# Kernel optimization log

Hardware: AMD Instinct MI355X
Metric: run time of the kernel (lower is better)

The kernel has to match this reference:

```python
import jax, jax.numpy as jnp
import numpy as np

B, C, H, W = 4, 512, 56, 56
G, K = 16, 3
P = K * K
GC = C // G
DWK = 3
PAD = 1
OFFSET_SCALE = 1.0


def setup_inputs():
    key = jax.random.key(0)
    ks = jax.random.split(key, 10)

    def w(i, shape, sc=0.02):
        return jax.random.normal(ks[i], shape, jnp.float32) * sc

    return {
        "x": jax.random.normal(ks[0], (B, C, H, W), jnp.float32),
        "w_in": w(1, (C, C)), "b_in": jnp.zeros((C,), jnp.float32),
        "w_dw": w(2, (DWK, DWK, 1, C)), "b_dw": jnp.zeros((C,), jnp.float32),
        "ln_g": jnp.ones((C,), jnp.float32), "ln_b": jnp.zeros((C,), jnp.float32),
        "w_off": w(3, (C, G * P * 2)), "b_off": jnp.zeros((G * P * 2,), jnp.float32),
        "w_mask": w(4, (C, G * P)), "b_mask": jnp.zeros((G * P,), jnp.float32),
        "w_out": w(5, (C, C)), "b_out": jnp.zeros((C,), jnp.float32),
        "bn_g": jnp.ones((C,), jnp.float32), "bn_b": jnp.zeros((C,), jnp.float32),
        "bn_m": w(6, (C,), 0.1), "bn_v": jnp.abs(w(7, (C,), 0.1)) + 1.0,
    }


def _dcnv3_core(xp, offset, mask):
    """xp: [B,H,W,C]; offset: [B,H,W,G*P*2]; mask (softmaxed over P): [B,H,W,G,P]."""
    xpad = jnp.pad(xp, ((0, 0), (PAD, PAD), (PAD, PAD), (0, 0)))
    Hin, Win = H + 2 * PAD, W + 2 * PAD
    # normalized reference points (output-location centers in padded input coords)
    ref_x = (jnp.arange(W, dtype=jnp.float32) + 0.5 + (K - 1) // 2) / Win
    ref_y = (jnp.arange(H, dtype=jnp.float32) + 0.5 + (K - 1) // 2) / Hin
    # dilation grid, kx-major / ky-minor flattening (matches InternImage core)
    k = jnp.arange(K, dtype=jnp.float32) - (K - 1) // 2
    gx = jnp.repeat(k, K) / Win  # [P]
    gy = jnp.tile(k, K) / Hin    # [P]
    off = offset.reshape(B, H, W, G, P, 2)
    lx = ref_x[None, None, :, None, None] + gx * OFFSET_SCALE + off[..., 0] * OFFSET_SCALE / Win
    ly = ref_y[None, :, None, None, None] + gy * OFFSET_SCALE + off[..., 1] * OFFSET_SCALE / Hin
    # grid_sample semantics, align_corners=False, zero padding
    px = lx * Win - 0.5
    py = ly * Hin - 0.5
    x0f = jnp.floor(px)
    y0f = jnp.floor(py)
    tx = px - x0f
    ty = py - y0f
    x0 = x0f.astype(jnp.int32)
    y0 = y0f.astype(jnp.int32)
    flat = xpad.reshape(B, Hin * Win * G, GC)
    gidx = jnp.arange(G)[None, None, :, None]

    def corner(fb, yi, xi):
        valid = (yi >= 0) & (yi < Hin) & (xi >= 0) & (xi < Win)
        idx = (jnp.clip(yi, 0, Hin - 1) * Win + jnp.clip(xi, 0, Win - 1)) * G + gidx
        return jnp.take(fb, idx, axis=0) * valid[..., None]  # [H,W,G,P,GC]

    def sample_one(fb, y0b, x0b, tyb, txb):
        w00 = ((1 - tyb) * (1 - txb))[..., None]
        w01 = ((1 - tyb) * txb)[..., None]
        w10 = (tyb * (1 - txb))[..., None]
        w11 = (tyb * txb)[..., None]
        return (corner(fb, y0b, x0b) * w00 + corner(fb, y0b, x0b + 1) * w01
                + corner(fb, y0b + 1, x0b) * w10 + corner(fb, y0b + 1, x0b + 1) * w11)

    samp = jax.vmap(sample_one)(flat, y0, x0, ty, tx)  # [B,H,W,G,P,GC]
    return jnp.einsum('bhwgpc,bhwgp->bhwgc', samp, mask).reshape(B, H, W, C)


def reference(x, w_in, b_in, w_dw, b_dw, ln_g, ln_b, w_off, b_off, w_mask, b_mask, w_out, b_out, bn_g, bn_b, bn_m, bn_v):
    xh = jnp.transpose(x, (0, 2, 3, 1))  # NCHW -> NHWC
    xp = xh @ w_in + b_in                # input_proj
    # offset/mask branch: depthwise conv + LayerNorm(channels) + GELU
    x1 = jax.lax.conv_general_dilated(xh, w_dw, (1, 1), 'SAME', feature_group_count=C,
                                      dimension_numbers=('NHWC', 'HWIO', 'NHWC')) + b_dw
    mu = x1.mean(-1, keepdims=True)
    var = x1.var(-1, keepdims=True)
    x1 = (x1 - mu) / jnp.sqrt(var + 1e-6) * ln_g + ln_b
    x1 = jax.nn.gelu(x1, approximate=False)
    offset = x1 @ w_off + b_off
    mask = jax.nn.softmax((x1 @ w_mask + b_mask).reshape(B, H, W, G, P), axis=-1)
    y = _dcnv3_core(xp, offset, mask)
    y = y @ w_out + b_out                # output_proj
    y = jnp.transpose(y, (0, 3, 1, 2))   # NHWC -> NCHW
    # BatchNorm2d (inference: running stats) + SiLU
    y = (y - bn_m[:, None, None]) / jnp.sqrt(bn_v[:, None, None] + 1e-5) * bn_g[:, None, None] + bn_b[:, None, None]
    return jax.nn.silu(y)
```

## Files before the change

### kernel.cpp

```cpp
#include <hip/hip_runtime.h>
#include <cmath>

constexpr int B_ = 4, C_ = 512, H_ = 56, W_ = 56;
constexpr int HW_ = H_ * W_;
constexpr int NPIX = B_ * HW_;
constexpr int G_ = 16, P_ = 9;
constexpr int NMSK = G_ * P_;
constexpr int GEMM_BLOCKS = 1568;
constexpr int TRANS_BLOCKS = (HW_ / 32) * (C_ / 32) * B_;
constexpr int PREP_BLOCKS = 16 * 16 * 3;

typedef __attribute__((ext_vector_type(8))) short short8;
typedef __attribute__((ext_vector_type(4))) float f32x4;

__device__ __forceinline__ float b2f(ushort u) {
    union { unsigned int i; float f; } v; v.i = (unsigned int)u << 16; return v.f;
}
__device__ __forceinline__ ushort f2b(float f) {
    unsigned int x = __float_as_uint(f);
    unsigned int r = (x + 0x7fffu + ((x >> 16) & 1u)) >> 16;
    return (ushort)r;
}
__device__ __forceinline__ void gload16(const ushort* g, ushort* l) {
    __builtin_amdgcn_global_load_lds(
        (const __attribute__((address_space(1))) unsigned int*)g,
        (__attribute__((address_space(3))) unsigned int*)l, 16, 0, 0);
}

union GemmSMem {
    struct { ushort As[64 * 64]; ushort Bs[64 * 64]; } s;
    float eb[64 * 67];
};

__global__ __launch_bounds__(256) void pre_kernel(
    const float* __restrict__ x, ushort* __restrict__ xh,
    const float* __restrict__ w_in, const float* __restrict__ w_off,
    const float* __restrict__ w_mask, const float* __restrict__ w_out,
    const float* __restrict__ b_off, const float* __restrict__ b_mask,
    ushort* __restrict__ wtA, ushort* __restrict__ wtOM, ushort* __restrict__ wtO,
    float* __restrict__ bOM)
{
    __shared__ float tile[32][33];
    int bid = blockIdx.x;
    int tx = threadIdx.x, ty = threadIdx.y;
    if (bid < TRANS_BLOCKS) {
        int bx = bid % 98;
        int rem = bid / 98;
        int by = rem % 16;
        int bz = rem / 16;
        int hw0 = bx * 32, c0 = by * 32;
        const float* ib = x + (size_t)bz * C_ * HW_;
        #pragma unroll
        for (int i = ty; i < 32; i += 8)
            tile[i][tx] = ib[(size_t)(c0 + i) * HW_ + hw0 + tx];
        __syncthreads();
        ushort* ob = xh + (size_t)bz * HW_ * C_;
        #pragma unroll
        for (int i = ty; i < 32; i += 8)
            ob[(size_t)(hw0 + i) * C_ + c0 + tx] = f2b(tile[tx][i]);
    } else {
        int p = bid - TRANS_BLOCKS;
        int px = p % 16;
        int py = (p / 16) % 16;
        int pz = p / 256;
        int k0 = px * 32;
        int n0 = py * 32;
        for (int i = ty; i < 32; i += 8) {
            int k = k0 + i, n = n0 + tx;
            float v;
            if (pz == 0) v = w_in[k * 512 + n];
            else if (pz == 1) v = w_out[k * 512 + n];
            else v = (n < 288) ? w_off[k * 288 + n]
                               : (n < 432 ? w_mask[k * 144 + (n - 288)] : 0.f);
            tile[i][tx] = v;
        }
        __syncthreads();
        ushort* dst = (pz == 0) ? wtA : (pz == 1 ? wtO : wtOM);
        for (int i = ty; i < 32; i += 8)
            dst[(size_t)(n0 + i) * 512 + k0 + tx] = f2b(tile[tx][i]);
        if (pz == 2 && px == 0 && py == 0) {
            int t = ty * 32 + tx;
            for (int tt = t; tt < 512; tt += 256)
                bOM[tt] = (tt < 288) ? b_off[tt] : (tt < 432 ? b_mask[tt - 288] : 0.f);
        }
    }
}

template <int MODE>
__device__ __forceinline__ void gemm_body(
    ushort* __restrict__ As, ushort* __restrict__ Bs, float* __restrict__ ebf,
    int wgid, const ushort* __restrict__ A, const ushort* __restrict__ Bt,
    const float* __restrict__ bias, void* __restrict__ Cout,
    const float* __restrict__ bng, const float* __restrict__ bnb,
    const float* __restrict__ bnm, const float* __restrict__ bnv)
{
    int tid = threadIdx.x;
    int lane = tid & 63, wid = tid >> 6;
    int row0 = (wgid >> 3) * 64, col0 = (wgid & 7) * 64;
    int wm = wid >> 1, wn = wid & 1;

    f32x4 acc[2][2] = {};

    int lr = lane >> 3;
    int sc = (lane & 7) ^ lr;

    for (int k0 = 0; k0 < 512; k0 += 64) {
        if (k0) __syncthreads();
        #pragma unroll
        for (int i = 0; i < 2; i++) {
            int s = wid * 2 + i;
            gload16(A + (size_t)(row0 + s * 8 + lr) * 512 + k0 + sc * 8, &As[s * 512]);
            gload16(Bt + (size_t)(col0 + s * 8 + lr) * 512 + k0 + sc * 8, &Bs[s * 512]);
        }
        __syncthreads();
        #pragma unroll
        for (int ks = 0; ks < 2; ks++) {
            short8 af[2], bf[2];
            #pragma unroll
            for (int mi = 0; mi < 2; mi++) {
                int r = wm * 32 + mi * 16 + (lane & 15);
                int c = ((lane >> 4) + ks * 4) ^ (r & 7);
                af[mi] = *(const short8*)((const char*)As + r * 128 + c * 16);
            }
            #pragma unroll
            for (int ni = 0; ni < 2; ni++) {
                int r = wn * 32 + ni * 16 + (lane & 15);
                int c = ((lane >> 4) + ks * 4) ^ (r & 7);
                bf[ni] = *(const short8*)((const char*)Bs + r * 128 + c * 16);
            }
            #pragma unroll
            for (int mi = 0; mi < 2; mi++)
                #pragma unroll
                for (int ni = 0; ni < 2; ni++)
                    acc[mi][ni] = __builtin_amdgcn_mfma_f32_16x16x32_bf16(
                        af[mi], bf[ni], acc[mi][ni], 0, 0, 0);
        }
    }

    if constexpr (MODE == 2) {
        __syncthreads();
        #pragma unroll
        for (int ni = 0; ni < 2; ni++) {
            int cl = wn * 32 + ni * 16 + (lane & 15);
            int col = col0 + cl;
            float bv = bias[col];
            float inv = rsqrtf(bnv[col] + 1e-5f);
            float bsc = bng[col] * inv;
            float bsh = bnb[col] - bnm[col] * bsc;
            int rl = (lane >> 4) * 4;
            #pragma unroll
            for (int mi = 0; mi < 2; mi++)
                #pragma unroll
                for (int r = 0; r < 4; r++) {
                    float val = acc[mi][ni][r] + bv;
                    float t2 = val * bsc + bsh;
                    float s = t2 / (1.f + expf(-t2));
                    ebf[cl * 67 + wm * 32 + mi * 16 + rl + r] = s;
                }
        }
        __syncthreads();
        int bb = row0 / HW_;
        int hw0 = row0 - bb * HW_;
        float* ob = (float*)Cout + (size_t)bb * C_ * HW_ + hw0 + lane;
        #pragma unroll
        for (int it = 0; it < 16; it++) {
            int chan = it * 4 + wid;
            ob[(size_t)(col0 + chan) * HW_] = ebf[chan * 67 + lane];
        }
    } else {
        #pragma unroll
        for (int ni = 0; ni < 2; ni++) {
            int col = col0 + wn * 32 + ni * 16 + (lane & 15);
            float bv = bias[col];
            #pragma unroll
            for (int mi = 0; mi < 2; mi++) {
                int rowb = row0 + wm * 32 + mi * 16 + (lane >> 4) * 4;
                #pragma unroll
                for (int r = 0; r < 4; r++) {
                    float val = acc[mi][ni][r] + bv;
                    if constexpr (MODE == 0)
                        ((float*)Cout)[(size_t)(rowb + r) * 512 + col] = val;
                    else
                        ((ushort*)Cout)[(size_t)(rowb + r) * 512 + col] = f2b(val);
                }
            }
        }
    }
}

template <int MODE, bool SKIPC7 = false>
__global__ __launch_bounds__(256) void mfma_gemm_kernel(
    const ushort* __restrict__ A, const ushort* __restrict__ Bt,
    const float* __restrict__ bias, void* __restrict__ Cout,
    const float* __restrict__ bng, const float* __restrict__ bnb,
    const float* __restrict__ bnm, const float* __restrict__ bnv)
{
    __shared__ GemmSMem sm;
    int bid = blockIdx.x;
    int wgid = (bid & 7) * (GEMM_BLOCKS / 8) + (bid >> 3);
    if (SKIPC7 && (wgid & 7) == 7) return;
    gemm_body<MODE>(sm.s.As, sm.s.Bs, sm.eb, wgid,
                    A, Bt, bias, Cout, bng, bnb, bnm, bnv);
}

__device__ __forceinline__ void dwln_body(
    int bid, const ushort* __restrict__ xh, const float* __restrict__ wdw,
    const float* __restrict__ bdw, const float* __restrict__ lng,
    const float* __restrict__ lnb, ushort* __restrict__ x1)
{
    int tid = threadIdx.x;
    int wid = tid >> 6, lane = tid & 63;
    int j = (bid & 7) * (NPIX / 32) + (bid >> 3);
    int n = j * 4 + wid;
    int b = n / HW_, hw = n % HW_;
    int h = hw / W_, w = hw % W_;
    int c0 = lane * 8;
    const ushort* base = xh + (size_t)b * HW_ * C_ + c0;

    uint4 nb[9];
    #pragma unroll
    for (int ky = 0; ky < 3; ky++)
        #pragma unroll
        for (int kx = 0; kx < 3; kx++) {
            int hh = h + ky - 1, ww = w + kx - 1;
            bool ok = (hh >= 0) & (hh < H_) & (ww >= 0) & (ww < W_);
            nb[ky * 3 + kx] = ok ? *(const uint4*)(base + ((size_t)hh * W_ + ww) * C_)
                                 : make_uint4(0u, 0u, 0u, 0u);
        }

    float acc[8];
    {
        float4 b0 = *(const float4*)&bdw[c0];
        float4 b1 = *(const float4*)&bdw[c0 + 4];
        acc[0] = b0.x; acc[1] = b0.y; acc[2] = b0.z; acc[3] = b0.w;
        acc[4] = b1.x; acc[5] = b1.y; acc[6] = b1.z; acc[7] = b1.w;
    }
    #pragma unroll
    for (int p = 0; p < 9; p++) {
        float4 w0 = *(const float4*)&wdw[p * C_ + c0];
        float4 w1 = *(const float4*)&wdw[p * C_ + c0 + 4];
        float wv[8] = {w0.x, w0.y, w0.z, w0.w, w1.x, w1.y, w1.z, w1.w};
        unsigned int u[4] = {nb[p].x, nb[p].y, nb[p].z, nb[p].w};
        #pragma unroll
        for (int q = 0; q < 4; q++) {
            float lo = __uint_as_float(u[q] << 16);
            float hi = __uint_as_float(u[q] & 0xffff0000u);
            acc[2 * q]     += wv[2 * q]     * lo;
            acc[2 * q + 1] += wv[2 * q + 1] * hi;
        }
    }

    float s1 = 0.f, s2 = 0.f;
    #pragma unroll
    for (int q = 0; q < 8; q++) { s1 += acc[q]; s2 += acc[q] * acc[q]; }
    #pragma unroll
    for (int o = 32; o > 0; o >>= 1) {
        s1 += __shfl_xor(s1, o);
        s2 += __shfl_xor(s2, o);
    }
    float mean = s1 * (1.f / 512.f);
    float var = s2 * (1.f / 512.f) - mean * mean;
    float inv = rsqrtf(var + 1e-6f);

    float4 g0 = *(const float4*)&lng[c0];
    float4 g1 = *(const float4*)&lng[c0 + 4];
    float4 e0 = *(const float4*)&lnb[c0];
    float4 e1 = *(const float4*)&lnb[c0 + 4];
    float gv[8] = {g0.x, g0.y, g0.z, g0.w, g1.x, g1.y, g1.z, g1.w};
    float ev[8] = {e0.x, e0.y, e0.z, e0.w, e1.x, e1.y, e1.z, e1.w};
    unsigned int outw[4];
    #pragma unroll
    for (int q = 0; q < 4; q++) {
        float t0 = (acc[2 * q]     - mean) * inv * gv[2 * q]     + ev[2 * q];
        float t1 = (acc[2 * q + 1] - mean) * inv * gv[2 * q + 1] + ev[2 * q + 1];
        float ge0 = 0.5f * t0 * (1.f + erff(t0 * 0.70710678118654752f));
        float ge1 = 0.5f * t1 * (1.f + erff(t1 * 0.70710678118654752f));
        outw[q] = (unsigned int)f2b(ge0) | ((unsigned int)f2b(ge1) << 16);
    }
    *(uint4*)&x1[(size_t)n * C_ + c0] = make_uint4(outw[0], outw[1], outw[2], outw[3]);
}

__global__ __launch_bounds__(256) void g1_dwln_kernel(
    const ushort* __restrict__ xh, const ushort* __restrict__ wtA,
    const float* __restrict__ b_in, ushort* __restrict__ xpb,
    const float* __restrict__ wdw, const float* __restrict__ bdw,
    const float* __restrict__ lng, const float* __restrict__ lnb,
    ushort* __restrict__ x1)
{
    __shared__ GemmSMem sm;
    int bid = blockIdx.x;
    if (bid < GEMM_BLOCKS) {
        int wgid = (bid & 7) * (GEMM_BLOCKS / 8) + (bid >> 3);
        gemm_body<1>(sm.s.As, sm.s.Bs, sm.eb, wgid,
                     xh, wtA, b_in, xpb, nullptr, nullptr, nullptr, nullptr);
    } else {
        dwln_body(bid - GEMM_BLOCKS, xh, wdw, bdw, lng, lnb, x1);
    }
}

__global__ __launch_bounds__(256) void dcn_sample_kernel(
    const ushort* __restrict__ xp, const ushort* __restrict__ om,
    ushort* __restrict__ y1)
{
    __shared__ float slog[NMSK];
    __shared__ float sw4[NMSK][4];
    __shared__ int   sa4[NMSK][4];
    int bid = blockIdx.x;
    int n = (bid & 7) * (NPIX / 8) + (bid >> 3);
    int b = n / HW_, hw = n % HW_;
    int h = hw / W_, w = hw % W_;
    int tid = threadIdx.x;
    const ushort* omp = om + (size_t)n * 512;

    if (tid < NMSK) slog[tid] = b2f(omp[288 + tid]);
    __syncthreads();
    if (tid < G_) {
        float mx = -1e30f;
        #pragma unroll
        for (int p = 0; p < P_; p++) mx = fmaxf(mx, slog[tid * P_ + p]);
        float e[P_], s = 0.f;
        #pragma unroll
        for (int p = 0; p < P_; p++) { e[p] = expf(slog[tid * P_ + p] - mx); s += e[p]; }
        float invs = 1.f / s;
        #pragma unroll
        for (int p = 0; p < P_; p++) slog[tid * P_ + p] = e[p] * invs;
    }
    __syncthreads();
    if (tid < NMSK) {
        int g = tid / 9, p = tid - g * 9;
        float ox = b2f(omp[g * 18 + p * 2 + 0]);
        float oy = b2f(omp[g * 18 + p * 2 + 1]);
        float px = (float)(w + (p / 3)) + ox;
        float py = (float)(h + (p % 3)) + oy;
        float x0f = floorf(px), y0f = floorf(py);
        float tx = px - x0f, ty = py - y0f;
        int x0 = (int)x0f, y0 = (int)y0f;
        float m = slog[tid];
        float ww[4] = { (1.f - ty) * (1.f - tx) * m, (1.f - ty) * tx * m,
                        ty * (1.f - tx) * m,         ty * tx * m };
        #pragma unroll
        for (int i = 0; i < 4; i++) {
            int yy = y0 + (i >> 1), xx = x0 + (i & 1);
            bool valid = (yy >= 1 && yy <= H_ && xx >= 1 && xx <= W_);
            sa4[tid][i] = valid ? ((yy - 1) * W_ + (xx - 1)) * C_ : 0;
            sw4[tid][i] = valid ? ww[i] : 0.f;
        }
    }
    __syncthreads();

    const ushort* xpb = xp + (size_t)b * HW_ * C_;
    int c0 = tid * 2;
    int g = tid >> 4;

    int addr[P_][4];
    #pragma unroll
    for (int p = 0; p < P_; p++)
        #pragma unroll
        for (int i = 0; i < 4; i++)
            addr[p][i] = sa4[g * 9 + p][i] + c0;

    unsigned int v[P_][4];
    #pragma unroll
    for (int p = 0; p < P_; p++)
        #pragma unroll
        for (int i = 0; i < 4; i++)
            v[p][i] = *(const unsigned int*)(xpb + addr[p][i]);

    float ax = 0.f, ay = 0.f;
    #pragma unroll
    for (int p = 0; p < P_; p++)
        #pragma unroll
        for (int i = 0; i < 4; i++) {
            float wgt = sw4[g * 9 + p][i];
            float lo = __uint_as_float(v[p][i] << 16);
            float hi = __uint_as_float(v[p][i] & 0xffff0000u);
            ax += wgt * lo;
            ay += wgt * hi;
        }

    ushort2 o; o.x = f2b(ax); o.y = f2b(ay);
    *(ushort2*)&y1[(size_t)n * 512 + c0] = o;
}

extern "C" void kernel_launch(void* const* d_in, const int* in_sizes, int n_in,
                              void* d_out, int out_size, void* d_ws, size_t ws_size,
                              hipStream_t stream)
{
    const float* x      = (const float*)d_in[0];
    const float* w_in   = (const float*)d_in[1];
    const float* b_in   = (const float*)d_in[2];
    const float* w_dw   = (const float*)d_in[3];
    const float* b_dw   = (const float*)d_in[4];
    const float* ln_g   = (const float*)d_in[5];
    const float* ln_b   = (const float*)d_in[6];
    const float* w_off  = (const float*)d_in[7];
    const float* b_off  = (const float*)d_in[8];
    const float* w_mask = (const float*)d_in[9];
    const float* b_mask = (const float*)d_in[10];
    const float* w_out  = (const float*)d_in[11];
    const float* b_out  = (const float*)d_in[12];
    const float* bn_g   = (const float*)d_in[13];
    const float* bn_b   = (const float*)d_in[14];
    const float* bn_m   = (const float*)d_in[15];
    const float* bn_v   = (const float*)d_in[16];
    float* out = (float*)d_out;

    const size_t NC = (size_t)NPIX * C_;
    char* wsp = (char*)d_ws;
    ushort* xh  = (ushort*)wsp;  wsp += NC * 2;
    ushort* x1  = (ushort*)wsp;  wsp += NC * 2;
    ushort* xpb = (ushort*)wsp;  wsp += NC * 2;
    ushort* om  = (ushort*)wsp;  wsp += NC * 2;
    ushort* wtA = (ushort*)wsp;  wsp += 512 * 512 * 2;
    ushort* wtOM= (ushort*)wsp;  wsp += 512 * 512 * 2;
    ushort* wtO = (ushort*)wsp;  wsp += 512 * 512 * 2;
    float*  bOM = (float*)wsp;   wsp += 512 * 4;

    dim3 tb(32, 8);
    pre_kernel<<<TRANS_BLOCKS + PREP_BLOCKS, tb, 0, stream>>>(
        x, xh, w_in, w_off, w_mask, w_out, b_off, b_mask, wtA, wtOM, wtO, bOM);

    g1_dwln_kernel<<<GEMM_BLOCKS + NPIX / 4, 256, 0, stream>>>(
        xh, wtA, b_in, xpb, w_dw, b_dw, ln_g, ln_b, x1);

    mfma_gemm_kernel<1, true><<<GEMM_BLOCKS, 256, 0, stream>>>(
        x1, wtOM, bOM, om, nullptr, nullptr, nullptr, nullptr);

    dcn_sample_kernel<<<NPIX, 256, 0, stream>>>(xpb, om, x1 );

    mfma_gemm_kernel<2><<<GEMM_BLOCKS, 256, 0, stream>>>(
        x1, wtO, b_out, out, bn_g, bn_b, bn_m, bn_v);
}
```

Baseline: 106.4 us.

## Process eight pixels per DCN sampling block with double-buffered gathers

The deformable sampling kernel now handles 8 consecutive pixels per block instead of one. The softmax and the bilinear weight/address setup run for all 8 pixels together, which cuts block count and launch/sync overhead. The gather loads for the next pixel pair are issued while the current pair is being accumulated, to hide memory latency. In exchange the kernel needs more shared memory and more registers (two 36-entry load buffers), which may lower occupancy.

```diff
diff --git a/kernel.cpp b/kernel.cpp
--- a/kernel.cpp
+++ b/kernel.cpp
@@ -9,6 +9,8 @@
 constexpr int GEMM_BLOCKS = 1568;
 constexpr int TRANS_BLOCKS = (HW_ / 32) * (C_ / 32) * B_;
 constexpr int PREP_BLOCKS = 16 * 16 * 3;
+constexpr int SPP = 8;
+constexpr int SAMP_BLOCKS = NPIX / SPP;
 
 typedef __attribute__((ext_vector_type(8))) short short8;
 typedef __attribute__((ext_vector_type(4))) float f32x4;
@@ -298,36 +300,72 @@
     }
 }
 
+__device__ __forceinline__ void samp_issue(
+    unsigned int (&v)[9][4], const ushort* __restrict__ xpb,
+    const int (*__restrict__ sa)[4], int c0)
+{
+    #pragma unroll
+    for (int p = 0; p < 9; p++)
+        #pragma unroll
+        for (int q = 0; q < 4; q++)
+            v[p][q] = *(const unsigned int*)(xpb + sa[p][q] + c0);
+}
+
+__device__ __forceinline__ void samp_accum(
+    const unsigned int (&v)[9][4], const float (*__restrict__ sw)[4],
+    ushort* __restrict__ y1, size_t outoff)
+{
+    float ax = 0.f, ay = 0.f;
+    #pragma unroll
+    for (int p = 0; p < 9; p++)
+        #pragma unroll
+        for (int q = 0; q < 4; q++) {
+            float wgt = sw[p][q];
+            ax += wgt * __uint_as_float(v[p][q] << 16);
+            ay += wgt * __uint_as_float(v[p][q] & 0xffff0000u);
+        }
+    ushort2 o; o.x = f2b(ax); o.y = f2b(ay);
+    *(ushort2*)&y1[outoff] = o;
+}
+
 __global__ __launch_bounds__(256) void dcn_sample_kernel(
     const ushort* __restrict__ xp, const ushort* __restrict__ om,
     ushort* __restrict__ y1)
 {
-    __shared__ float slog[NMSK];
-    __shared__ float sw4[NMSK][4];
-    __shared__ int   sa4[NMSK][4];
+    __shared__ float slog[SPP][NMSK];
+    __shared__ float sw4[SPP][NMSK][4];
+    __shared__ int   sa4[SPP][NMSK][4];
     int bid = blockIdx.x;
-    int n = (bid & 7) * (NPIX / 8) + (bid >> 3);
-    int b = n / HW_, hw = n % HW_;
-    int h = hw / W_, w = hw % W_;
+    int j = (bid & 7) * (SAMP_BLOCKS / 8) + (bid >> 3);
+    int n_base = j * SPP;
+    int b = n_base / HW_;
+    int hwb = n_base - b * HW_;
     int tid = threadIdx.x;
-    const ushort* omp = om + (size_t)n * 512;
-
-    if (tid < NMSK) slog[tid] = b2f(omp[288 + tid]);
+
+    for (int i = tid; i < SPP * NMSK; i += 256) {
+        int pp = i / NMSK, idx = i - pp * NMSK;
+        slog[pp][idx] = b2f(om[(size_t)(n_base + pp) * 512 + 288 + idx]);
+    }
     __syncthreads();
-    if (tid < G_) {
+    if (tid < SPP * G_) {
+        int pp = tid >> 4, g = tid & 15;
         float mx = -1e30f;
         #pragma unroll
-        for (int p = 0; p < P_; p++) mx = fmaxf(mx, slog[tid * P_ + p]);
+        for (int p = 0; p < P_; p++) mx = fmaxf(mx, slog[pp][g * P_ + p]);
         float e[P_], s = 0.f;
         #pragma unroll
-        for (int p = 0; p < P_; p++) { e[p] = expf(slog[tid * P_ + p] - mx); s += e[p]; }
+        for (int p = 0; p < P_; p++) { e[p] = expf(slog[pp][g * P_ + p] - mx); s += e[p]; }
         float invs = 1.f / s;
         #pragma unroll
-        for (int p = 0; p < P_; p++) slog[tid * P_ + p] = e[p] * invs;
+        for (int p = 0; p < P_; p++) slog[pp][g * P_ + p] = e[p] * invs;
     }
     __syncthreads();
-    if (tid < NMSK) {
-        int g = tid / 9, p = tid - g * 9;
+    for (int i = tid; i < SPP * NMSK; i += 256) {
+        int pp = i / NMSK, t = i - pp * NMSK;
+        int g = t / 9, p = t - g * 9;
+        int hw = hwb + pp;
+        int h = hw / W_, w = hw - h * W_;
+        const ushort* omp = om + (size_t)(n_base + pp) * 512;
         float ox = b2f(omp[g * 18 + p * 2 + 0]);
         float oy = b2f(omp[g * 18 + p * 2 + 1]);
         float px = (float)(w + (p / 3)) + ox;
@@ -335,51 +373,32 @@
         float x0f = floorf(px), y0f = floorf(py);
         float tx = px - x0f, ty = py - y0f;
         int x0 = (int)x0f, y0 = (int)y0f;
-        float m = slog[tid];
+        float m = slog[pp][t];
         float ww[4] = { (1.f - ty) * (1.f - tx) * m, (1.f - ty) * tx * m,
                         ty * (1.f - tx) * m,         ty * tx * m };
         #pragma unroll
-        for (int i = 0; i < 4; i++) {
-            int yy = y0 + (i >> 1), xx = x0 + (i & 1);
+        for (int q = 0; q < 4; q++) {
+            int yy = y0 + (q >> 1), xx = x0 + (q & 1);
             bool valid = (yy >= 1 && yy <= H_ && xx >= 1 && xx <= W_);
-            sa4[tid][i] = valid ? ((yy - 1) * W_ + (xx - 1)) * C_ : 0;
-            sw4[tid][i] = valid ? ww[i] : 0.f;
+            sa4[pp][t][q] = valid ? ((yy - 1) * W_ + (xx - 1)) * C_ : 0;
+            sw4[pp][t][q] = valid ? ww[q] : 0.f;
         }
     }
     __syncthreads();
 
+    int g = tid >> 4;
+    int c0 = tid * 2;
     const ushort* xpb = xp + (size_t)b * HW_ * C_;
-    int c0 = tid * 2;
-    int g = tid >> 4;
-
-    int addr[P_][4];
-    #pragma unroll
-    for (int p = 0; p < P_; p++)
-        #pragma unroll
-        for (int i = 0; i < 4; i++)
-            addr[p][i] = sa4[g * 9 + p][i] + c0;
-
-    unsigned int v[P_][4];
-    #pragma unroll
-    for (int p = 0; p < P_; p++)
-        #pragma unroll
-        for (int i = 0; i < 4; i++)
-            v[p][i] = *(const unsigned int*)(xpb + addr[p][i]);
-
-    float ax = 0.f, ay = 0.f;
-    #pragma unroll
-    for (int p = 0; p < P_; p++)
-        #pragma unroll
-        for (int i = 0; i < 4; i++) {
-            float wgt = sw4[g * 9 + p][i];
-            float lo = __uint_as_float(v[p][i] << 16);
-            float hi = __uint_as_float(v[p][i] & 0xffff0000u);
-            ax += wgt * lo;
-            ay += wgt * hi;
-        }
-
-    ushort2 o; o.x = f2b(ax); o.y = f2b(ay);
-    *(ushort2*)&y1[(size_t)n * 512 + c0] = o;
+    unsigned int v0[9][4], v1[9][4];
+    samp_issue(v0, xpb, &sa4[0][g * 9], c0);
+    samp_issue(v1, xpb, &sa4[1][g * 9], c0);
+    #pragma unroll
+    for (int pp = 0; pp < SPP; pp += 2) {
+        samp_accum(v0, &sw4[pp][g * 9], y1, (size_t)(n_base + pp) * 512 + c0);
+        if (pp + 2 < SPP) samp_issue(v0, xpb, &sa4[pp + 2][g * 9], c0);
+        samp_accum(v1, &sw4[pp + 1][g * 9], y1, (size_t)(n_base + pp + 1) * 512 + c0);
+        if (pp + 3 < SPP) samp_issue(v1, xpb, &sa4[pp + 3][g * 9], c0);
+    }
 }
 
 extern "C" void kernel_launch(void* const* d_in, const int* in_sizes, int n_in,
@@ -426,7 +445,7 @@
     mfma_gemm_kernel<1, true><<<GEMM_BLOCKS, 256, 0, stream>>>(
         x1, wtOM, bOM, om, nullptr, nullptr, nullptr, nullptr);
 
-    dcn_sample_kernel<<<NPIX, 256, 0, stream>>>(xpb, om, x1 );
+    dcn_sample_kernel<<<SAMP_BLOCKS, 256, 0, stream>>>(xpb, om, x1 );
 
     mfma_gemm_kernel<2><<<GEMM_BLOCKS, 256, 0, stream>>>(
         x1, wtO, b_out, out, bn_g, bn_b, bn_m, bn_v);
```

After: 114.8 us. 1.08x slower.
